# Kernel tuning notes

Hardware: AMD Instinct MI355X
Metric: run time of the kernel (lower is better)

The kernel has to match this reference:

```python
import jax, jax.numpy as jnp
import numpy as np
import math

B, L, H, E = 16, 1024, 8, 64   # L = nsensor = N (forced by einsum 'bhls,bhlg')
WIN = 1024                      # win_size, last dim of x
G = 64                          # n_group
D_SEL = 1                       # d_sel default


def setup_inputs() -> dict:
    key = jax.random.key(0)
    ks = jax.random.split(key, 7)
    return {
        "queries": jax.random.normal(ks[0], (B, L, H, E), dtype=jnp.float32),
        "keys": jax.random.normal(ks[1], (B, L, H, E), dtype=jnp.float32),
        "values": jax.random.normal(ks[2], (B, L, H, E), dtype=jnp.float32),
        "x": jax.random.normal(ks[3], (B, L, WIN), dtype=jnp.float32),
        "mlp_w": jax.random.normal(ks[4], (H * D_SEL, WIN), dtype=jnp.float32) * 0.02,
        "mlp_b": jax.random.normal(ks[5], (H * D_SEL,), dtype=jnp.float32) * 0.02,
        "sel_W": jax.random.normal(ks[6], (H, G, D_SEL), dtype=jnp.float32),
        "attn_mask": 0,
    }


def _select_attention(x, mlp_w, mlp_b, sel_W, n_heads, d_sel):
    b, n, lwin = x.shape
    xf = x.reshape(b * n, lwin)
    newx = jnp.tanh(xf @ mlp_w.T + mlp_b)                 # [(B*N), H*d_sel]
    # Faithful raw reshape (torch.reshape, no permute): mixes n and h axes.
    newx = newx.reshape(b, n_heads, n, d_sel)             # [B, H, N, d_sel]
    sel = jnp.einsum('bhnd,hgd->bhng', newx, sel_W)       # [B, H, N, G]
    return jax.nn.relu(sel)


def reference(queries, keys, values, x, mlp_w, mlp_b, sel_W, attn_mask):
    b, l, h, e = queries.shape
    scale = 1.0 / math.sqrt(e)
    scores = jnp.einsum('blhe,bshe->bhls', queries, keys)      # [B, H, L, S]
    sel = _select_attention(x, mlp_w, mlp_b, sel_W, h, D_SEL)  # [B, H, L, G]
    scores = jnp.einsum('bhls,bhlg->bhsg', scores, sel)        # [B, H, S, G]
    series = jax.nn.softmax(scale * scores, axis=-1)           # softmax over groups
    # values labeled 'blhs': l=S (value len), s=D (feature). Output V: [B, D, H, G]
    V = jnp.einsum('blhs,bhlg->bshg', values, series)
    return V
```

## Files before the change

kernel.cpp:

```cpp
#include <hip/hip_runtime.h>
#include <math.h>

#define NB 16
#define NL 1024
#define NH 8
#define NE 64
#define NWIN 1024
#define NG 64

#define SCH 128
#define SROW 136

typedef __attribute__((ext_vector_type(8))) short short8;
typedef __attribute__((ext_vector_type(4))) float floatx4;

__device__ __forceinline__ short f2bf(float x) {
    unsigned u = __float_as_uint(x);
    u += 0x7fffu + ((u >> 16) & 1u);
    return (short)(u >> 16);
}
__device__ __forceinline__ float dot4(float4 a, float4 b) {
    return fmaf(a.x, b.x, fmaf(a.y, b.y, fmaf(a.z, b.z, a.w * b.w)));
}

__global__ __launch_bounds__(256, 4) void k_sel_q(
    const float* __restrict__ x, const float* __restrict__ mlp_w,
    const float* __restrict__ mlp_b, const float* __restrict__ q,
    float* __restrict__ qp, float* __restrict__ qn)
{
    __shared__ float4 w_lds[8][NWIN / 4];
    __shared__ float t_lds[128];
    __shared__ float redp[4][64], redn[4][64];

    int tid = threadIdx.x;
    int blk = blockIdx.x;
    int ee = blk & 7, bh = blk >> 3;
    int b = bh >> 3, h = bh & 7;
    int w = tid >> 6, lane = tid & 63;
    int sq = lane >> 4, c = lane & 15;

    const float4* w4 = (const float4*)mlp_w;
    float4* wl = (float4*)w_lds;
    #pragma unroll
    for (int i = 0; i < 8; ++i)
        wl[tid + 256 * i] = w4[tid + 256 * i];
    __syncthreads();

    int row_loc = w * 4 + sq;
    int r = b * 1024 + h * 128 + ee * 16 + row_loc;
    const float4* xr = (const float4*)(x + (size_t)r * NWIN);
    float4 a03 = make_float4(0,0,0,0), a47 = make_float4(0,0,0,0);
    #pragma unroll
    for (int i = 0; i < 16; ++i) {
        float4 xv = xr[i * 16 + c];
        a03.x += dot4(xv, w_lds[0][i * 16 + c]);
        a03.y += dot4(xv, w_lds[1][i * 16 + c]);
        a03.z += dot4(xv, w_lds[2][i * 16 + c]);
        a03.w += dot4(xv, w_lds[3][i * 16 + c]);
        a47.x += dot4(xv, w_lds[4][i * 16 + c]);
        a47.y += dot4(xv, w_lds[5][i * 16 + c]);
        a47.z += dot4(xv, w_lds[6][i * 16 + c]);
        a47.w += dot4(xv, w_lds[7][i * 16 + c]);
    }
    #pragma unroll
    for (int off = 1; off < 16; off <<= 1) {
        a03.x += __shfl_xor(a03.x, off, 64);
        a03.y += __shfl_xor(a03.y, off, 64);
        a03.z += __shfl_xor(a03.z, off, 64);
        a03.w += __shfl_xor(a03.w, off, 64);
        a47.x += __shfl_xor(a47.x, off, 64);
        a47.y += __shfl_xor(a47.y, off, 64);
        a47.z += __shfl_xor(a47.z, off, 64);
        a47.w += __shfl_xor(a47.w, off, 64);
    }
    if (c == 0) {
        float4 b03 = *(const float4*)mlp_b;
        float4 b47 = *(const float4*)(mlp_b + 4);
        float4 t03, t47;
        t03.x = tanhf(a03.x + b03.x); t03.y = tanhf(a03.y + b03.y);
        t03.z = tanhf(a03.z + b03.z); t03.w = tanhf(a03.w + b03.w);
        t47.x = tanhf(a47.x + b47.x); t47.y = tanhf(a47.y + b47.y);
        t47.z = tanhf(a47.z + b47.z); t47.w = tanhf(a47.w + b47.w);
        *(float4*)&t_lds[row_loc * 8]     = t03;
        *(float4*)&t_lds[row_loc * 8 + 4] = t47;
    }
    __syncthreads();

    int lo = sq, e4 = c;
    float4 accp = make_float4(0,0,0,0), accn = make_float4(0,0,0,0);
    #pragma unroll
    for (int i = 0; i < 8; ++i) {
        int l_loc = w * 32 + i * 4 + lo;
        float tv = t_lds[l_loc];
        int l = ee * 128 + l_loc;
        float4 qv = *(const float4*)(q + (((size_t)(b * NL + l)) * NH + h) * NE + e4 * 4);
        float tp = fmaxf(tv, 0.f), tn = fminf(tv, 0.f);
        accp.x = fmaf(tp, qv.x, accp.x); accp.y = fmaf(tp, qv.y, accp.y);
        accp.z = fmaf(tp, qv.z, accp.z); accp.w = fmaf(tp, qv.w, accp.w);
        accn.x = fmaf(tn, qv.x, accn.x); accn.y = fmaf(tn, qv.y, accn.y);
        accn.z = fmaf(tn, qv.z, accn.z); accn.w = fmaf(tn, qv.w, accn.w);
    }
    #pragma unroll
    for (int off = 16; off <= 32; off <<= 1) {
        accp.x += __shfl_xor(accp.x, off, 64); accp.y += __shfl_xor(accp.y, off, 64);
        accp.z += __shfl_xor(accp.z, off, 64); accp.w += __shfl_xor(accp.w, off, 64);
        accn.x += __shfl_xor(accn.x, off, 64); accn.y += __shfl_xor(accn.y, off, 64);
        accn.z += __shfl_xor(accn.z, off, 64); accn.w += __shfl_xor(accn.w, off, 64);
    }
    if (lo == 0) {
        *(float4*)&redp[w][e4 * 4] = accp;
        *(float4*)&redn[w][e4 * 4] = accn;
    }
    __syncthreads();
    if (tid < 64) {
        atomicAdd(&qp[bh * NE + tid], redp[0][tid] + redp[1][tid] + redp[2][tid] + redp[3][tid]);
    } else if (tid < 128) {
        int e = tid - 64;
        atomicAdd(&qn[bh * NE + e], redn[0][e] + redn[1][e] + redn[2][e] + redn[3][e]);
    }
}

__global__ __launch_bounds__(256, 4) void k_attn_out(
    const float* __restrict__ keys, const float* __restrict__ values,
    const float* __restrict__ sel_W,
    const float* __restrict__ qp, const float* __restrict__ qn,
    float* __restrict__ out)
{
    __shared__ short sb[NG][SROW];
    __shared__ float ap_l[SCH], an_l[SCH];
    __shared__ float2 wpn[NG];
    __shared__ float mx2[2][SCH], dn2[2][SCH];

    int tid = threadIdx.x, blk = blockIdx.x;
    int chunk = blk & 7, bh = blk >> 3;
    int b = bh >> 3, h = bh & 7;
    int w = tid >> 6, lane = tid & 63;
    int c = lane & 15, sq = lane >> 4;
    const float scale = 0.125f;

    if (tid < NG) {
        float W = sel_W[h * NG + tid];
        wpn[tid] = make_float2(fmaxf(W, 0.f) * scale, fminf(W, 0.f) * scale);
    }

    const float4 qp4 = *(const float4*)(qp + bh * NE + c * 4);
    const float4 qn4 = *(const float4*)(qn + bh * NE + c * 4);
    int s0 = chunk * SCH;

    #pragma unroll
    for (int p = 0; p < 8; ++p) {
        int sl = w * 32 + p * 4 + sq;
        float4 kv = *(const float4*)(keys + (((size_t)(b * NL + s0 + sl)) * NH + h) * NE + c * 4);
        float pp = dot4(kv, qp4);
        float pn = dot4(kv, qn4);
        #pragma unroll
        for (int m_ = 1; m_ <= 8; m_ <<= 1) {
            pp += __shfl_xor(pp, m_, 64);
            pn += __shfl_xor(pn, m_, 64);
        }
        if (c == 0) { ap_l[sl] = pp; an_l[sl] = pn; }
    }
    __syncthreads();

    {
        int s_ = tid & 127, gh = tid >> 7, g0 = gh * 32;
        float ap = ap_l[s_], an = an_l[s_];
        float m = -1e30f;
        #pragma unroll 8
        for (int g = 0; g < 32; ++g) {
            float2 wv = wpn[g0 + g];
            m = fmaxf(m, fmaf(wv.x, ap, wv.y * an));
        }
        mx2[gh][s_] = m;
        __syncthreads();
        m = fmaxf(mx2[0][s_], mx2[1][s_]);
        float d = 0.f;
        #pragma unroll 8
        for (int g = 0; g < 32; ++g) {
            float2 wv = wpn[g0 + g];
            d += __expf(fmaf(wv.x, ap, wv.y * an) - m);
        }
        dn2[gh][s_] = d;
        __syncthreads();
        float inv = 1.0f / (dn2[0][s_] + dn2[1][s_]);
        #pragma unroll 8
        for (int g = 0; g < 32; ++g) {
            float2 wv = wpn[g0 + g];
            sb[g0 + g][s_] = f2bf(__expf(fmaf(wv.x, ap, wv.y * an) - m) * inv);
        }
    }
    __syncthreads();

    floatx4 acc[4] = {{0.f,0.f,0.f,0.f},{0.f,0.f,0.f,0.f},
                      {0.f,0.f,0.f,0.f},{0.f,0.f,0.f,0.f}};
    const float* vbase = values + (((size_t)(b * NL + s0)) * NH + h) * NE + 16 * w + c;
    #pragma unroll
    for (int ks = 0; ks < 4; ++ks) {
        float a[8];
        #pragma unroll
        for (int j = 0; j < 8; ++j)
            a[j] = vbase[(size_t)(ks * 32 + sq * 8 + j) * (NH * NE)];
        short8 av;
        #pragma unroll
        for (int j = 0; j < 8; ++j) av[j] = f2bf(a[j]);
        #pragma unroll
        for (int n = 0; n < 4; ++n) {
            short8 bv = *(const short8*)&sb[16 * n + c][ks * 32 + sq * 8];
            acc[n] = __builtin_amdgcn_mfma_f32_16x16x32_bf16(av, bv, acc[n], 0, 0, 0);
        }
    }

    #pragma unroll
    for (int n = 0; n < 4; ++n) {
        #pragma unroll
        for (int r = 0; r < 4; ++r) {
            int e = 16 * w + sq * 4 + r;
            int g = 16 * n + c;
            atomicAdd(&out[((size_t)(b * NE + e) * NH + h) * NG + g], acc[n][r]);
        }
    }
}

extern "C" void kernel_launch(void* const* d_in, const int* in_sizes, int n_in,
                              void* d_out, int out_size, void* d_ws, size_t ws_size,
                              hipStream_t stream) {
    (void)in_sizes; (void)n_in; (void)ws_size;
    const float* queries = (const float*)d_in[0];
    const float* keys    = (const float*)d_in[1];
    const float* values  = (const float*)d_in[2];
    const float* x       = (const float*)d_in[3];
    const float* mlp_w   = (const float*)d_in[4];
    const float* mlp_b   = (const float*)d_in[5];
    const float* sel_W   = (const float*)d_in[6];
    float* out = (float*)d_out;

    float* qp_ws = (float*)d_ws;
    float* qn_ws = qp_ws + NB * NH * NE;

    hipMemsetAsync(out, 0, (size_t)out_size * sizeof(float), stream);
    hipMemsetAsync(qp_ws, 0, (size_t)2 * NB * NH * NE * sizeof(float), stream);

    k_sel_q<<<dim3(NB * NH * 8), dim3(256), 0, stream>>>(x, mlp_w, mlp_b,
                                                          queries, qp_ws, qn_ws);
    k_attn_out<<<dim3(NB * NH * 8), dim3(256), 0, stream>>>(keys, values, sel_W,
                                                            qp_ws, qn_ws, out);
}
```

Measured before the change: 203.2 us.

## Prefetch values tile into LDS asynchronously during softmax computation

The values chunk is issued as direct global-to-LDS loads at kernel start, so the transfer overlaps the key dot-products and softmax work. The MFMA stage then reads from LDS, using an XOR swizzle to avoid bank conflicts, instead of issuing strided scalar global loads. __syncthreads is replaced by an lgkmcnt wait plus s_barrier so the pending vector-memory loads are not drained early. This adds 32KB of LDS per block, which may reduce occupancy below the 4 blocks per CU requested by launch bounds.

```diff
diff --git a/kernel.cpp b/kernel.cpp
--- a/kernel.cpp
+++ b/kernel.cpp
@@ -21,6 +21,17 @@
 }
 __device__ __forceinline__ float dot4(float4 a, float4 b) {
     return fmaf(a.x, b.x, fmaf(a.y, b.y, fmaf(a.z, b.z, a.w * b.w)));
+}
+
+__device__ __forceinline__ void lgkm_barrier() {
+    asm volatile("s_waitcnt lgkmcnt(0)" ::: "memory");
+    __builtin_amdgcn_s_barrier();
+}
+
+__device__ __forceinline__ void gl_lds16(const float* g, float* l) {
+    __builtin_amdgcn_global_load_lds(
+        (const __attribute__((address_space(1))) float*)g,
+        (__attribute__((address_space(3))) float*)l, 16, 0, 0);
 }
 
 __global__ __launch_bounds__(256, 4) void k_sel_q(
@@ -127,9 +138,10 @@
     float* __restrict__ out)
 {
     __shared__ short sb[NG][SROW];
+    __shared__ float vst[4][2048];
     __shared__ float ap_l[SCH], an_l[SCH];
     __shared__ float2 wpn[NG];
-    __shared__ float mx2[2][SCH], dn2[2][SCH];
+    __shared__ float mxdn[2][SCH];
 
     int tid = threadIdx.x, blk = blockIdx.x;
     int chunk = blk & 7, bh = blk >> 3;
@@ -137,6 +149,17 @@
     int w = tid >> 6, lane = tid & 63;
     int c = lane & 15, sq = lane >> 4;
     const float scale = 0.125f;
+    int s0 = chunk * SCH;
+
+    {
+        float* vstW = &vst[w][0];
+        int s_loc = (lane >> 2) ^ ((lane >> 5) & 1);
+        const float* vsrc = values + (((size_t)(b * NL + s0 + s_loc)) * NH + h) * NE
+                          + 16 * w + 4 * (lane & 3);
+        #pragma unroll
+        for (int i = 0; i < 8; ++i)
+            gl_lds16(vsrc + (size_t)(16 * i) * (NH * NE), vstW + 256 * i);
+    }
 
     if (tid < NG) {
         float W = sel_W[h * NG + tid];
@@ -145,7 +168,6 @@
 
     const float4 qp4 = *(const float4*)(qp + bh * NE + c * 4);
     const float4 qn4 = *(const float4*)(qn + bh * NE + c * 4);
-    int s0 = chunk * SCH;
 
     #pragma unroll
     for (int p = 0; p < 8; ++p) {
@@ -160,7 +182,7 @@
         }
         if (c == 0) { ap_l[sl] = pp; an_l[sl] = pn; }
     }
-    __syncthreads();
+    lgkm_barrier();
 
     {
         int s_ = tid & 127, gh = tid >> 7, g0 = gh * 32;
@@ -171,38 +193,42 @@
             float2 wv = wpn[g0 + g];
             m = fmaxf(m, fmaf(wv.x, ap, wv.y * an));
         }
-        mx2[gh][s_] = m;
-        __syncthreads();
-        m = fmaxf(mx2[0][s_], mx2[1][s_]);
+        mxdn[gh][s_] = m;
+        lgkm_barrier();
+        m = fmaxf(mxdn[0][s_], mxdn[1][s_]);
+        lgkm_barrier();
         float d = 0.f;
         #pragma unroll 8
         for (int g = 0; g < 32; ++g) {
             float2 wv = wpn[g0 + g];
             d += __expf(fmaf(wv.x, ap, wv.y * an) - m);
         }
-        dn2[gh][s_] = d;
-        __syncthreads();
-        float inv = 1.0f / (dn2[0][s_] + dn2[1][s_]);
+        mxdn[gh][s_] = d;
+        lgkm_barrier();
+        float inv = 1.0f / (mxdn[0][s_] + mxdn[1][s_]);
         #pragma unroll 8
         for (int g = 0; g < 32; ++g) {
             float2 wv = wpn[g0 + g];
             sb[g0 + g][s_] = f2bf(__expf(fmaf(wv.x, ap, wv.y * an) - m) * inv);
         }
     }
-    __syncthreads();
+    lgkm_barrier();
+
+    asm volatile("s_waitcnt vmcnt(0)" ::: "memory");
+    __builtin_amdgcn_sched_barrier(0);
 
     floatx4 acc[4] = {{0.f,0.f,0.f,0.f},{0.f,0.f,0.f,0.f},
                       {0.f,0.f,0.f,0.f},{0.f,0.f,0.f,0.f}};
-    const float* vbase = values + (((size_t)(b * NL + s0)) * NH + h) * NE + 16 * w + c;
+    const float* vstW = &vst[w][0];
+    int sq1 = sq & 1;
     #pragma unroll
     for (int ks = 0; ks < 4; ++ks) {
-        float a[8];
-        #pragma unroll
-        for (int j = 0; j < 8; ++j)
-            a[j] = vbase[(size_t)(ks * 32 + sq * 8 + j) * (NH * NE)];
         short8 av;
         #pragma unroll
-        for (int j = 0; j < 8; ++j) av[j] = f2bf(a[j]);
+        for (int j = 0; j < 8; ++j) {
+            int slot = (ks * 32 + sq * 8 + j) ^ sq1;
+            av[j] = f2bf(vstW[slot * 16 + c]);
+        }
         #pragma unroll
         for (int n = 0; n < 4; ++n) {
             short8 bv = *(const short8*)&sb[16 * n + c][ks * 32 + sq * 8];
```

Result: slower. 211.4 us (+4.1%).

## Prefetch keys and values early and use LDS-only barriers in attn_out

Applied to the files above, without the earlier changes.

Issues all key loads up front and prefetches the values tile into registers, split in two halves, before the softmax phase. Global value loads can then overlap the score and softmax computation instead of stalling the MFMA loop. Replaces __syncthreads with a barrier that waits only on LDS counters, so the in-flight global loads do not block the barriers. This raises register pressure, which under launch_bounds(256,4) may cause spills.

```diff
diff --git a/kernel.cpp b/kernel.cpp
--- a/kernel.cpp
+++ b/kernel.cpp
@@ -21,6 +21,11 @@
 }
 __device__ __forceinline__ float dot4(float4 a, float4 b) {
     return fmaf(a.x, b.x, fmaf(a.y, b.y, fmaf(a.z, b.z, a.w * b.w)));
+}
+
+__device__ __forceinline__ void lgkm_barrier() {
+    asm volatile("s_waitcnt lgkmcnt(0)" ::: "memory");
+    __builtin_amdgcn_s_barrier();
 }
 
 __global__ __launch_bounds__(256, 4) void k_sel_q(
@@ -137,22 +142,34 @@
     int w = tid >> 6, lane = tid & 63;
     int c = lane & 15, sq = lane >> 4;
     const float scale = 0.125f;
-
+    int s0 = chunk * SCH;
+
+    const float4 qp4 = *(const float4*)(qp + bh * NE + c * 4);
+    const float4 qn4 = *(const float4*)(qn + bh * NE + c * 4);
     if (tid < NG) {
         float W = sel_W[h * NG + tid];
         wpn[tid] = make_float2(fmaxf(W, 0.f) * scale, fminf(W, 0.f) * scale);
     }
 
-    const float4 qp4 = *(const float4*)(qp + bh * NE + c * 4);
-    const float4 qn4 = *(const float4*)(qn + bh * NE + c * 4);
-    int s0 = chunk * SCH;
-
+    float4 kvv[8];
     #pragma unroll
     for (int p = 0; p < 8; ++p) {
         int sl = w * 32 + p * 4 + sq;
-        float4 kv = *(const float4*)(keys + (((size_t)(b * NL + s0 + sl)) * NH + h) * NE + c * 4);
-        float pp = dot4(kv, qp4);
-        float pn = dot4(kv, qn4);
+        kvv[p] = *(const float4*)(keys + (((size_t)(b * NL + s0 + sl)) * NH + h) * NE + c * 4);
+    }
+
+    const float* vbase = values + (((size_t)(b * NL + s0)) * NH + h) * NE + 16 * w + c;
+    float vregA[16];
+    #pragma unroll
+    for (int m = 0; m < 16; ++m)
+        vregA[m] = vbase[(size_t)((m >> 3) * 32 + sq * 8 + (m & 7)) * (NH * NE)];
+    __builtin_amdgcn_sched_barrier(0);
+
+    #pragma unroll
+    for (int p = 0; p < 8; ++p) {
+        int sl = w * 32 + p * 4 + sq;
+        float pp = dot4(kvv[p], qp4);
+        float pn = dot4(kvv[p], qn4);
         #pragma unroll
         for (int m_ = 1; m_ <= 8; m_ <<= 1) {
             pp += __shfl_xor(pp, m_, 64);
@@ -160,7 +177,14 @@
         }
         if (c == 0) { ap_l[sl] = pp; an_l[sl] = pn; }
     }
-    __syncthreads();
+
+    float vregB[16];
+    #pragma unroll
+    for (int m = 0; m < 16; ++m)
+        vregB[m] = vbase[(size_t)((2 + (m >> 3)) * 32 + sq * 8 + (m & 7)) * (NH * NE)];
+    __builtin_amdgcn_sched_barrier(0);
+
+    lgkm_barrier();
 
     {
         int s_ = tid & 127, gh = tid >> 7, g0 = gh * 32;
@@ -172,7 +196,7 @@
             m = fmaxf(m, fmaf(wv.x, ap, wv.y * an));
         }
         mx2[gh][s_] = m;
-        __syncthreads();
+        lgkm_barrier();
         m = fmaxf(mx2[0][s_], mx2[1][s_]);
         float d = 0.f;
         #pragma unroll 8
@@ -181,7 +205,7 @@
             d += __expf(fmaf(wv.x, ap, wv.y * an) - m);
         }
         dn2[gh][s_] = d;
-        __syncthreads();
+        lgkm_barrier();
         float inv = 1.0f / (dn2[0][s_] + dn2[1][s_]);
         #pragma unroll 8
         for (int g = 0; g < 32; ++g) {
@@ -189,20 +213,16 @@
             sb[g0 + g][s_] = f2bf(__expf(fmaf(wv.x, ap, wv.y * an) - m) * inv);
         }
     }
-    __syncthreads();
+    lgkm_barrier();
 
     floatx4 acc[4] = {{0.f,0.f,0.f,0.f},{0.f,0.f,0.f,0.f},
                       {0.f,0.f,0.f,0.f},{0.f,0.f,0.f,0.f}};
-    const float* vbase = values + (((size_t)(b * NL + s0)) * NH + h) * NE + 16 * w + c;
     #pragma unroll
     for (int ks = 0; ks < 4; ++ks) {
-        float a[8];
+        short8 av;
         #pragma unroll
         for (int j = 0; j < 8; ++j)
-            a[j] = vbase[(size_t)(ks * 32 + sq * 8 + j) * (NH * NE)];
-        short8 av;
-        #pragma unroll
-        for (int j = 0; j < 8; ++j) av[j] = f2bf(a[j]);
+            av[j] = f2bf(ks < 2 ? vregA[ks * 8 + j] : vregB[(ks - 2) * 8 + j]);
         #pragma unroll
         for (int n = 0; n < 4; ++n) {
             short8 bv = *(const short8*)&sb[16 * n + c][ks * 32 + sq * 8];
```

Measured after the change: 198.9 us. 1.02x faster.
